# Kernel optimization log

Hardware: AMD Instinct MI355X
Metric: run time of the kernel (lower is better)

The kernel has to match this reference:

```python
import jax, jax.numpy as jnp
import numpy as np

N = 50000      # nodes
E = 800000     # edges
F = 64         # num_features
H = 64         # hidden_channels
L = 3          # num_layers
C0 = 16        # conv1d_channels[0]
TOTAL = H * L + 1  # 193, concat dim / Conv1d kernel size


def setup_inputs() -> dict:
    key = jax.random.key(0)
    ks = jax.random.split(key, 13)
    s = 0.05
    x = jax.random.normal(ks[0], (N, F), jnp.float32)
    edge_index = jax.random.randint(ks[1], (2, E), 0, N)
    edge_attr = jax.random.normal(ks[2], (E, 1), jnp.float32)
    W0 = jax.random.normal(ks[3], (F, H), jnp.float32) * s
    b0 = jnp.zeros((H,), jnp.float32)
    W1 = jax.random.normal(ks[4], (H, H), jnp.float32) * s
    b1 = jnp.zeros((H,), jnp.float32)
    W2 = jax.random.normal(ks[5], (H, H), jnp.float32) * s
    b2 = jnp.zeros((H,), jnp.float32)
    W3 = jax.random.normal(ks[6], (H, 1), jnp.float32) * s
    b3 = jnp.zeros((1,), jnp.float32)
    conv_w = jax.random.normal(ks[7], (C0, TOTAL), jnp.float32) * s  # Conv1d(1,C0,K=TOTAL,stride=TOTAL) weight squeezed
    conv_b = jnp.zeros((C0,), jnp.float32)
    return dict(x=x, edge_index=edge_index, edge_attr=edge_attr,
                W0=W0, b0=b0, W1=W1, b1=b1, W2=W2, b2=b2, W3=W3, b3=b3,
                conv_w=conv_w, conv_b=conv_b)


def _gcn(h, W, b, src, dst, norm):
    # PyG GCNConv: h' = segsum_dst(norm * (h W)[src]) + b
    h = h @ W                                   # [N, out]
    msg = h[src] * norm[:, None]                # [E+N, out] gather (irregular)
    out = jax.ops.segment_sum(msg, dst, num_segments=N)
    return out + b


def reference(x, edge_index, edge_attr, W0, b0, W1, b1, W2, b2, W3, b3, conv_w, conv_b):
    del edge_attr  # use_edge_attr=False
    loops = jnp.arange(N, dtype=edge_index.dtype)
    src = jnp.concatenate([edge_index[0], loops])  # add self-loops
    dst = jnp.concatenate([edge_index[1], loops])
    deg = jax.ops.segment_sum(jnp.ones_like(dst, dtype=x.dtype), dst, num_segments=N)
    dinv = jax.lax.rsqrt(jnp.maximum(deg, 1.0))
    norm = dinv[src] * dinv[dst]

    xs = []
    h = x
    for W, b in ((W0, b0), (W1, b1), (W2, b2), (W3, b3)):
        h = _gcn(h, W, b, src, dst, norm)
        xs.append(h)
    cat = jnp.concatenate(xs, axis=-1)           # [N, TOTAL] (k=1 drops input x)
    # Conv1d(1, C0, K=TOTAL, stride=TOTAL) over length-TOTAL signal == dense projection
    out = cat @ conv_w.T + conv_b                # [N, C0]
    return out
```

## Files before the change

kernel.cpp:

```cpp
#include <hip/hip_runtime.h>
#include <math.h>

static constexpr int N    = 50000;
static constexpr int E    = 800000;
static constexpr int NC   = 16;
static constexpr int TOT  = 193;
static constexpr int NB   = (N + 255) / 256;
static constexpr int DP   = 16;

static constexpr int KQ1 = 0;
static constexpr int KQ2 = 1024;
static constexpr int KQ3 = 2048;
static constexpr int KV  = 3072;
static constexpr int KU1 = 3136;
static constexpr int KU2 = 3152;
static constexpr int KD  = 3168;
static constexpr int KSC = 3184;
static constexpr int KSZ = 3200;

__device__ __forceinline__ unsigned short f2bf(float f) {
    union { float f; unsigned int i; } v; v.f = f;
    unsigned int b = v.i + 0x7FFFu + ((v.i >> 16) & 1u);
    return (unsigned short)(b >> 16);
}


__global__ void k_count(const int* __restrict__ dst, int* __restrict__ degp,
                        int* __restrict__ pos) {
    int e = blockIdx.x * blockDim.x + threadIdx.x;
    if (e < E / 4) {
        int d0 = dst[e], d1 = dst[e + E / 4];
        int d2 = dst[e + E / 2], d3 = dst[e + 3 * E / 4];
        int p0 = atomicAdd(&degp[d0 * DP], 1);
        int p1 = atomicAdd(&degp[d1 * DP], 1);
        int p2 = atomicAdd(&degp[d2 * DP], 1);
        int p3 = atomicAdd(&degp[d3 * DP], 1);
        pos[e] = p0;
        pos[e + E / 4] = p1;
        pos[e + E / 2] = p2;
        pos[e + 3 * E / 4] = p3;
    }
}

__global__ __launch_bounds__(256) void k_part(const int* __restrict__ degp,
                                              int* __restrict__ part) {
    __shared__ int red[256];
    const int t = threadIdx.x;
    int i = blockIdx.x * 256 + t;
    int v = (i < N) ? (degp[i * DP] + 1) : 0;
    red[t] = v;
    __syncthreads();
#pragma unroll
    for (int off = 128; off; off >>= 1) {
        if (t < off) red[t] += red[t + off];
        __syncthreads();
    }
    if (t == 0) part[blockIdx.x] = red[0];
}

__global__ __launch_bounds__(256) void k_scatter(const int* __restrict__ degp,
                                                 const int* __restrict__ part,
                                                 int* __restrict__ row_ptr,
                                                 float* __restrict__ dinv,
                                                 int2* __restrict__ edges) {
    __shared__ int s[256];
    __shared__ int red[256];
    const int t = threadIdx.x;
    const int bid = blockIdx.x;
    red[t] = (t < bid && t < NB) ? part[t] : 0;
    __syncthreads();
#pragma unroll
    for (int off = 128; off; off >>= 1) {
        if (t < off) red[t] += red[t + off];
        __syncthreads();
    }
    const int base = red[0];

    int i = bid * 256 + t;
    int v = (i < N) ? (degp[i * DP] + 1) : 0;
    s[t] = v;
    __syncthreads();
#pragma unroll
    for (int off = 1; off < 256; off <<= 1) {
        int u = (t >= off) ? s[t - off] : 0;
        __syncthreads();
        s[t] += u;
        __syncthreads();
    }
    if (i < N) {
        int rp = base + s[t] - v;
        row_ptr[i] = rp;
        float dv = rsqrtf((float)v);
        dinv[i] = dv;
        edges[rp] = make_int2(i, __float_as_int(dv * dv));
        if (i == N - 1) row_ptr[N] = base + s[t];
    }
}

__global__ void k_fill(const int* __restrict__ src, const int* __restrict__ dst,
                       const int* __restrict__ pos,
                       const int* __restrict__ row_ptr,
                       const float* __restrict__ dinv,
                       int2* __restrict__ edges) {
    int idx = blockIdx.x * blockDim.x + threadIdx.x;
    if (idx < E) {
        int s = src[idx], d = dst[idx];
        int p = row_ptr[d] + 1 + pos[idx];
        edges[p] = make_int2(s, __float_as_int(dinv[s] * dinv[d]));
    }
}

__global__ __launch_bounds__(256) void k_xbf(const float* __restrict__ x,
                                             ushort* __restrict__ xb,
                                             int* __restrict__ degp) {
    int i = blockIdx.x * 256 + threadIdx.x;
    if (i * 4 >= N * 64) return;
    degp[i] = 0;
    float4 v = ((const float4*)x)[i];
    ushort4 o;
    o.x = f2bf(v.x); o.y = f2bf(v.y); o.z = f2bf(v.z); o.w = f2bf(v.w);
    ((ushort4*)xb)[i] = o;
}

__global__ __launch_bounds__(256) void k_setup(
    const float* __restrict__ W0, const float* __restrict__ b0,
    const float* __restrict__ W1, const float* __restrict__ b1,
    const float* __restrict__ W2, const float* __restrict__ b2,
    const float* __restrict__ W3, const float* __restrict__ b3,
    const float* __restrict__ cw, const float* __restrict__ cb,
    float* __restrict__ K) {
    __shared__ float W0s[4096], W1s[4096], W2s[4096], P2s[4096];
    __shared__ float C1[1024], C2[1024], C3[1024], R3s[1024];
    __shared__ float W3s[64], b0s[64], b1s[64], b2s[64];
    __shared__ float r3[64], rb1[64], rb2[64], rb12[64];
    const int t = threadIdx.x;
    const int k = t >> 2, q = t & 3;

    for (int i = t; i < 4096; i += 256) {
        W0s[i] = W0[i]; W1s[i] = W1[i]; W2s[i] = W2[i];
    }
    for (int i = t; i < 1024; i += 256) {
        int j = i >> 4, c = i & 15;
        C1[i] = cw[c * TOT + j];
        C2[i] = cw[c * TOT + 64 + j];
        C3[i] = cw[c * TOT + 128 + j];
    }
    if (t < 64) { W3s[t] = W3[t]; b0s[t] = b0[t]; b1s[t] = b1[t]; b2s[t] = b2[t]; }
    __syncthreads();

    {
        const int j0 = q * 16;
        float acc[16];
#pragma unroll
        for (int jj = 0; jj < 16; ++jj) acc[jj] = 0.f;
        for (int m = 0; m < 64; ++m) {
            float w = W0s[k * 64 + m];
#pragma unroll
            for (int jj = 0; jj < 16; ++jj) acc[jj] += w * W1s[m * 64 + j0 + jj];
        }
#pragma unroll
        for (int jj = 0; jj < 16; ++jj) P2s[k * 64 + j0 + jj] = acc[jj];
    }
    {
        const int c0 = q * 4;
        float acc[4] = {0.f, 0.f, 0.f, 0.f};
        for (int j = 0; j < 64; ++j) {
            float w = W2s[k * 64 + j];
#pragma unroll
            for (int cc = 0; cc < 4; ++cc) acc[cc] += w * C3[j * 16 + c0 + cc];
        }
#pragma unroll
        for (int cc = 0; cc < 4; ++cc) R3s[k * 16 + c0 + cc] = acc[cc];
    }
    if (q == 0) {
        float a = 0.f;
        for (int j = 0; j < 64; ++j) a += W2s[k * 64 + j] * W3s[j];
        r3[k] = a;
    }
    if (q == 1) {
        float a = 0.f;
        for (int m = 0; m < 64; ++m) a += b0s[m] * W1s[m * 64 + k];
        rb1[k] = a;
    }
    if (q == 2) {
        float a = 0.f;
        for (int m = 0; m < 64; ++m) a += b1s[m] * W2s[m * 64 + k];
        rb2[k] = a;
    }
    __syncthreads();

    {
        const int c0 = q * 4;
        float q1[4] = {0,0,0,0}, q2[4] = {0,0,0,0}, q3[4] = {0,0,0,0};
        for (int j = 0; j < 64; ++j) {
            float w0 = W0s[k * 64 + j], p2 = P2s[k * 64 + j];
#pragma unroll
            for (int cc = 0; cc < 4; ++cc) {
                q1[cc] += w0 * C1[j * 16 + c0 + cc];
                q2[cc] += p2 * C2[j * 16 + c0 + cc];
                q3[cc] += p2 * R3s[j * 16 + c0 + cc];
            }
        }
#pragma unroll
        for (int cc = 0; cc < 4; ++cc) {
            K[KQ1 + k * 16 + c0 + cc] = q1[cc];
            K[KQ2 + k * 16 + c0 + cc] = q2[cc];
            K[KQ3 + k * 16 + c0 + cc] = q3[cc];
        }
    }
    if (q == 3) {
        float a = 0.f;
        for (int j = 0; j < 64; ++j) a += P2s[k * 64 + j] * r3[j];
        K[KV + k] = a;
    }
    if (q == 0) {
        float a = 0.f;
        for (int m = 0; m < 64; ++m) a += rb1[m] * W2s[m * 64 + k];
        rb12[k] = a;
    }
    __syncthreads();

    if (t < 16) {
        float a1 = 0.f, a2 = 0.f, ad = 0.f;
        for (int j = 0; j < 64; ++j) {
            a1 += rb1[j] * C2[j * 16 + t] + rb2[j] * C3[j * 16 + t];
            a2 += rb12[j] * C3[j * 16 + t];
            ad += b0s[j] * C1[j * 16 + t] + b1s[j] * C2[j * 16 + t]
                + b2s[j] * C3[j * 16 + t];
        }
        K[KU1 + t] = a1; K[KU2 + t] = a2; K[KD + t] = ad + cb[t];
    }
    if (t == 0) {
        float al = 0.f, be = 0.f, ga = 0.f;
        for (int j = 0; j < 64; ++j) {
            al += rb12[j] * W3s[j]; be += rb2[j] * W3s[j]; ga += b2s[j] * W3s[j];
        }
        K[KSC + 0] = al; K[KSC + 1] = be; K[KSC + 2] = ga;
    }
}

template <int LAYER>
__global__ __launch_bounds__(256) void k_layer(
    const ushort* __restrict__ Min,
    const int2* __restrict__ edges,
    const int* __restrict__ row_ptr,
    const float* __restrict__ K,
    const float* __restrict__ s1in,
    const float* __restrict__ s2in,
    ushort* __restrict__ Mout,
    float* __restrict__ s_out,
    float* __restrict__ t4,
    float* __restrict__ out) {
    __shared__ float QT[64 * 17];
    const int tid = threadIdx.x;
    constexpr int KQ = (LAYER == 0) ? KQ1 : (LAYER == 1) ? KQ2 : KQ3;
    for (int i = tid; i < 1024; i += 256) {
        int j = i >> 4, c = i & 15;
        QT[j * 17 + c] = K[KQ + i];
    }
    const int lane = tid & 63;
    const int w    = tid >> 6;
    const int q    = lane >> 4;
    const int m    = lane & 15;
    float v0 = 0.f, v1 = 0.f, v2 = 0.f, v3 = 0.f;
    if constexpr (LAYER == 2) {
        v0 = K[KV + 4 * m + 0]; v1 = K[KV + 4 * m + 1];
        v2 = K[KV + 4 * m + 2]; v3 = K[KV + 4 * m + 3];
    }
    __syncthreads();

    const int nn = blockIdx.x * 16 + w * 4 + q;
    const int rp0 = row_ptr[nn], rp1 = row_ptr[nn + 1];
    const int d = rp1 - rp0;
    int dmax = max(d, __shfl_xor(d, 16));
    dmax = max(dmax, __shfl_xor(dmax, 32));
    const int trips = __builtin_amdgcn_readfirstlane((dmax + 7) >> 3);

    float a0 = 0.f, a1 = 0.f, a2 = 0.f, a3 = 0.f, accs = 0.f;
    for (int t = 0; t < trips; ++t) {
        const int base = rp0 + t * 8;
        int col[8]; float wv[8];
#pragma unroll
        for (int i = 0; i < 8; ++i) {
            int pi = base + i;
            int pc = min(pi, rp1 - 1);
            int2 e = edges[pc];
            col[i] = e.x;
            wv[i] = (pi < rp1) ? __int_as_float(e.y) : 0.f;
        }
        unsigned long long g[8];
#pragma unroll
        for (int i = 0; i < 8; ++i)
            g[i] = *(const unsigned long long*)(Min + col[i] * 64 + 4 * m);
        if constexpr (LAYER == 0) {
#pragma unroll
            for (int i = 0; i < 8; ++i) accs += wv[i];
        }
#pragma unroll
        for (int i = 0; i < 8; ++i) {
            unsigned int lo = (unsigned int)g[i];
            unsigned int hi = (unsigned int)(g[i] >> 32);
            union { unsigned int u; float f; } x0, x1, x2, x3;
            x0.u = lo << 16; x1.u = lo & 0xFFFF0000u;
            x2.u = hi << 16; x3.u = hi & 0xFFFF0000u;
            a0 += wv[i] * x0.f; a1 += wv[i] * x1.f;
            a2 += wv[i] * x2.f; a3 += wv[i] * x3.f;
        }
    }

    if constexpr (LAYER < 2) {
        unsigned long long pk =
              (unsigned long long)f2bf(a0)
            | ((unsigned long long)f2bf(a1) << 16)
            | ((unsigned long long)f2bf(a2) << 32)
            | ((unsigned long long)f2bf(a3) << 48);
        ((unsigned long long*)Mout)[nn * 16 + m] = pk;
    }
    if constexpr (LAYER == 0) {
        if (m == 0) s_out[nn] = accs;
    }
    if constexpr (LAYER == 1) {
        float ss = 0.f;
        for (int p = rp0 + m; p < rp1; p += 16) {
            int2 e = edges[p];
            ss += __int_as_float(e.y) * s1in[e.x];
        }
        ss += __shfl_xor(ss, 1); ss += __shfl_xor(ss, 2);
        ss += __shfl_xor(ss, 4); ss += __shfl_xor(ss, 8);
        if (m == 0) s_out[nn] = ss;
    }

    float s1n = 0.f, s2n = 0.f;
    if constexpr (LAYER == 2) {
        s1n = s1in[nn]; s2n = s2in[nn];
        float tv = a0 * v0 + a1 * v1 + a2 * v2 + a3 * v3;
        tv += __shfl_xor(tv, 1); tv += __shfl_xor(tv, 2);
        tv += __shfl_xor(tv, 4); tv += __shfl_xor(tv, 8);
        if (m == 0)
            t4[nn] = tv + K[KSC + 0] * s2n + K[KSC + 1] * s1n + K[KSC + 2];
    }

    float r = 0.f;
#pragma unroll
    for (int a = 0; a < 16; ++a) {
        int srcl = (q << 4) + a;
        float f0 = __shfl(a0, srcl), f1 = __shfl(a1, srcl);
        float f2 = __shfl(a2, srcl), f3 = __shfl(a3, srcl);
        r += f0 * QT[(4 * a + 0) * 17 + m] + f1 * QT[(4 * a + 1) * 17 + m]
           + f2 * QT[(4 * a + 2) * 17 + m] + f3 * QT[(4 * a + 3) * 17 + m];
    }
    {
        int o = nn * NC + m;
        if constexpr (LAYER == 0) {
            out[o] = K[KD + m] + r;
        } else if constexpr (LAYER == 1) {
            out[o] += r;
        } else {
            out[o] += r + s1n * K[KU1 + m] + s2n * K[KU2 + m];
        }
    }
}

__global__ __launch_bounds__(256) void k_agg4_out(
    const float* __restrict__ t4, const int2* __restrict__ edges,
    const int* __restrict__ row_ptr, const float* __restrict__ b3,
    const float* __restrict__ conv_w, float* __restrict__ out) {
    int n = blockIdx.x * blockDim.x + threadIdx.x;
    if (n >= N) return;
    int p0 = row_ptr[n], p1 = row_ptr[n + 1];
    float a0 = 0.f, a1 = 0.f;
    for (int p = p0; p < p1; p += 4) {
        int q0 = min(p, p1 - 1), q1 = min(p + 1, p1 - 1);
        int q2 = min(p + 2, p1 - 1), q3 = min(p + 3, p1 - 1);
        int2 e0 = edges[q0], e1 = edges[q1], e2 = edges[q2], e3 = edges[q3];
        float w0 = __int_as_float(e0.y);
        float w1 = (p + 1 < p1) ? __int_as_float(e1.y) : 0.f;
        float w2 = (p + 2 < p1) ? __int_as_float(e2.y) : 0.f;
        float w3 = (p + 3 < p1) ? __int_as_float(e3.y) : 0.f;
        a0 += w0 * t4[e0.x]; a1 += w1 * t4[e1.x];
        a0 += w2 * t4[e2.x]; a1 += w3 * t4[e3.x];
    }
    float h4 = a0 + a1 + b3[0];
    float4* o4 = (float4*)(out + n * NC);
#pragma unroll
    for (int k = 0; k < 4; ++k) {
        float4 v = o4[k];
        v.x += h4 * conv_w[(4 * k + 0) * TOT + 192];
        v.y += h4 * conv_w[(4 * k + 1) * TOT + 192];
        v.z += h4 * conv_w[(4 * k + 2) * TOT + 192];
        v.w += h4 * conv_w[(4 * k + 3) * TOT + 192];
        o4[k] = v;
    }
}


extern "C" void kernel_launch(void* const* d_in, const int* in_sizes, int n_in,
                              void* d_out, int out_size, void* d_ws, size_t ws_size,
                              hipStream_t stream) {
    const float* x   = (const float*)d_in[0];
    const int*   ei  = (const int*)d_in[1];
    const int*   src = ei;
    const int*   dst = ei + E;
    const float* W0  = (const float*)d_in[3];
    const float* b0  = (const float*)d_in[4];
    const float* W1  = (const float*)d_in[5];
    const float* b1  = (const float*)d_in[6];
    const float* W2  = (const float*)d_in[7];
    const float* b2  = (const float*)d_in[8];
    const float* W3  = (const float*)d_in[9];
    const float* b3  = (const float*)d_in[10];
    const float* cw  = (const float*)d_in[11];
    const float* cb  = (const float*)d_in[12];
    float* out = (float*)d_out;

    char* p = (char*)d_ws;
    auto alloc = [&](size_t nbytes) {
        char* r = p;
        p += (nbytes + 255) & ~(size_t)255;
        return (void*)r;
    };
    int*    degp    = (int*)alloc((size_t)N * DP * 4);
    int*    pos     = (int*)alloc((size_t)E * 4);
    int*    row_ptr = (int*)alloc((size_t)(N + 1) * 4);
    float*  dinv    = (float*)alloc((size_t)N * 4);
    int*    part    = (int*)alloc((size_t)NB * 4);
    int2*   edges   = (int2*)alloc((size_t)(E + N) * 8);
    ushort* xb      = (ushort*)alloc((size_t)N * 64 * 2);
    ushort* M1      = (ushort*)alloc((size_t)N * 64 * 2);
    ushort* M2      = (ushort*)alloc((size_t)N * 64 * 2);
    float*  s1      = (float*)alloc((size_t)N * 4);
    float*  s2      = (float*)alloc((size_t)N * 4);
    float*  t4      = (float*)alloc((size_t)N * 4);
    float*  K       = (float*)alloc((size_t)KSZ * 4);

    k_setup<<<1, 256, 0, stream>>>(W0, b0, W1, b1, W2, b2, W3, b3, cw, cb, K);
    k_xbf<<<(N * 64 / 4 + 255) / 256, 256, 0, stream>>>(x, xb, degp);

    k_count  <<<(E / 4 + 255) / 256, 256, 0, stream>>>(dst, degp, pos);
    k_part   <<<NB, 256, 0, stream>>>(degp, part);
    k_scatter<<<NB, 256, 0, stream>>>(degp, part, row_ptr, dinv, edges);
    k_fill   <<<(E + 255) / 256, 256, 0, stream>>>(src, dst, pos, row_ptr, dinv, edges);

    const int layerGrid = N / 16;

    k_layer<0><<<layerGrid, 256, 0, stream>>>(
        xb, edges, row_ptr, K, nullptr, nullptr, M1, s1, nullptr, out);
    k_layer<1><<<layerGrid, 256, 0, stream>>>(
        M1, edges, row_ptr, K, s1, nullptr, M2, s2, nullptr, out);
    k_layer<2><<<layerGrid, 256, 0, stream>>>(
        M2, edges, row_ptr, K, s1, s2, nullptr, nullptr, t4, out);
    k_agg4_out<<<(N + 255) / 256, 256, 0, stream>>>(t4, edges, row_ptr, b3, cw, out);
}
```

Before: 175.4 us.

## Split bf16 feature matrices into two 32-column halves processed by separate launches

Stores the node feature matrices as two separate 32-column bf16 halves. Each layer now runs as two kernel passes, one per half, so each gather touches a 3.2 MB array that may stay resident in cache better than the original 6.4 MB one. Each wave handles 8 nodes with 8 lanes instead of 4 nodes with 16 lanes. The cost is reading the edge list twice per layer, twice as many launches, and extra read-modify-write traffic on the output and t4.

```diff
diff --git a/kernel.cpp b/kernel.cpp
--- a/kernel.cpp
+++ b/kernel.cpp
@@ -111,7 +111,8 @@
 }
 
 __global__ __launch_bounds__(256) void k_xbf(const float* __restrict__ x,
-                                             ushort* __restrict__ xb,
+                                             ushort* __restrict__ xbA,
+                                             ushort* __restrict__ xbB,
                                              int* __restrict__ degp) {
     int i = blockIdx.x * 256 + threadIdx.x;
     if (i * 4 >= N * 64) return;
@@ -119,7 +120,9 @@
     float4 v = ((const float4*)x)[i];
     ushort4 o;
     o.x = f2bf(v.x); o.y = f2bf(v.y); o.z = f2bf(v.z); o.w = f2bf(v.w);
-    ((ushort4*)xb)[i] = o;
+    int n = i >> 4, q16 = i & 15;
+    if (q16 < 8) ((ushort4*)xbA)[n * 8 + q16] = o;
+    else         ((ushort4*)xbB)[n * 8 + (q16 - 8)] = o;
 }
 
 __global__ __launch_bounds__(256) void k_setup(
@@ -239,7 +242,7 @@
     }
 }
 
-template <int LAYER>
+template <int LAYER, int HALF>
 __global__ __launch_bounds__(256) void k_layer(
     const ushort* __restrict__ Min,
     const int2* __restrict__ edges,
@@ -251,28 +254,33 @@
     float* __restrict__ s_out,
     float* __restrict__ t4,
     float* __restrict__ out) {
-    __shared__ float QT[64 * 17];
+    __shared__ float QT[32 * 17];
     const int tid = threadIdx.x;
     constexpr int KQ = (LAYER == 0) ? KQ1 : (LAYER == 1) ? KQ2 : KQ3;
-    for (int i = tid; i < 1024; i += 256) {
+    for (int i = tid; i < 512; i += 256) {
         int j = i >> 4, c = i & 15;
-        QT[j * 17 + c] = K[KQ + i];
+        QT[j * 17 + c] = K[KQ + (HALF * 32 + j) * 16 + c];
     }
     const int lane = tid & 63;
     const int w    = tid >> 6;
-    const int q    = lane >> 4;
-    const int m    = lane & 15;
+    const int oct  = lane >> 3;
+    const int m8   = lane & 7;
     float v0 = 0.f, v1 = 0.f, v2 = 0.f, v3 = 0.f;
     if constexpr (LAYER == 2) {
-        v0 = K[KV + 4 * m + 0]; v1 = K[KV + 4 * m + 1];
-        v2 = K[KV + 4 * m + 2]; v3 = K[KV + 4 * m + 3];
-    }
-    __syncthreads();
-
-    const int nn = blockIdx.x * 16 + w * 4 + q;
-    const int rp0 = row_ptr[nn], rp1 = row_ptr[nn + 1];
+        v0 = K[KV + HALF * 32 + 4 * m8 + 0];
+        v1 = K[KV + HALF * 32 + 4 * m8 + 1];
+        v2 = K[KV + HALF * 32 + 4 * m8 + 2];
+        v3 = K[KV + HALF * 32 + 4 * m8 + 3];
+    }
+    __syncthreads();
+
+    const int nn = blockIdx.x * 32 + w * 8 + oct;
+    const bool valid = nn < N;
+    int rp0 = 0, rp1 = 1;
+    if (valid) { rp0 = row_ptr[nn]; rp1 = row_ptr[nn + 1]; }
     const int d = rp1 - rp0;
-    int dmax = max(d, __shfl_xor(d, 16));
+    int dmax = max(d, __shfl_xor(d, 8));
+    dmax = max(dmax, __shfl_xor(dmax, 16));
     dmax = max(dmax, __shfl_xor(dmax, 32));
     const int trips = __builtin_amdgcn_readfirstlane((dmax + 7) >> 3);
 
@@ -291,8 +299,8 @@
         unsigned long long g[8];
 #pragma unroll
         for (int i = 0; i < 8; ++i)
-            g[i] = *(const unsigned long long*)(Min + col[i] * 64 + 4 * m);
-        if constexpr (LAYER == 0) {
+            g[i] = *(const unsigned long long*)(Min + col[i] * 32 + 4 * m8);
+        if constexpr (LAYER == 0 && HALF == 0) {
 #pragma unroll
             for (int i = 0; i < 8; ++i) accs += wv[i];
         }
@@ -309,54 +317,66 @@
     }
 
     if constexpr (LAYER < 2) {
-        unsigned long long pk =
-              (unsigned long long)f2bf(a0)
-            | ((unsigned long long)f2bf(a1) << 16)
-            | ((unsigned long long)f2bf(a2) << 32)
-            | ((unsigned long long)f2bf(a3) << 48);
-        ((unsigned long long*)Mout)[nn * 16 + m] = pk;
-    }
-    if constexpr (LAYER == 0) {
-        if (m == 0) s_out[nn] = accs;
-    }
-    if constexpr (LAYER == 1) {
+        if (valid) {
+            unsigned long long pk =
+                  (unsigned long long)f2bf(a0)
+                | ((unsigned long long)f2bf(a1) << 16)
+                | ((unsigned long long)f2bf(a2) << 32)
+                | ((unsigned long long)f2bf(a3) << 48);
+            ((unsigned long long*)Mout)[nn * 8 + m8] = pk;
+        }
+    }
+    if constexpr (LAYER == 0 && HALF == 0) {
+        if (m8 == 0 && valid) s_out[nn] = accs;
+    }
+    if constexpr (LAYER == 1 && HALF == 0) {
         float ss = 0.f;
-        for (int p = rp0 + m; p < rp1; p += 16) {
+        for (int p = rp0 + m8; p < rp1; p += 8) {
             int2 e = edges[p];
             ss += __int_as_float(e.y) * s1in[e.x];
         }
         ss += __shfl_xor(ss, 1); ss += __shfl_xor(ss, 2);
-        ss += __shfl_xor(ss, 4); ss += __shfl_xor(ss, 8);
-        if (m == 0) s_out[nn] = ss;
+        ss += __shfl_xor(ss, 4);
+        if (m8 == 0 && valid) s_out[nn] = ss;
     }
 
     float s1n = 0.f, s2n = 0.f;
     if constexpr (LAYER == 2) {
-        s1n = s1in[nn]; s2n = s2in[nn];
+        int nc = valid ? nn : 0;
+        s1n = s1in[nc]; s2n = s2in[nc];
         float tv = a0 * v0 + a1 * v1 + a2 * v2 + a3 * v3;
         tv += __shfl_xor(tv, 1); tv += __shfl_xor(tv, 2);
-        tv += __shfl_xor(tv, 4); tv += __shfl_xor(tv, 8);
-        if (m == 0)
-            t4[nn] = tv + K[KSC + 0] * s2n + K[KSC + 1] * s1n + K[KSC + 2];
-    }
-
-    float r = 0.f;
-#pragma unroll
-    for (int a = 0; a < 16; ++a) {
-        int srcl = (q << 4) + a;
+        tv += __shfl_xor(tv, 4);
+        if (m8 == 0 && valid) {
+            if constexpr (HALF == 0)
+                t4[nn] = tv + K[KSC + 0] * s2n + K[KSC + 1] * s1n + K[KSC + 2];
+            else
+                t4[nn] += tv;
+        }
+    }
+
+    float r0 = 0.f, r1 = 0.f;
+#pragma unroll
+    for (int a = 0; a < 8; ++a) {
+        int srcl = (oct << 3) + a;
         float f0 = __shfl(a0, srcl), f1 = __shfl(a1, srcl);
         float f2 = __shfl(a2, srcl), f3 = __shfl(a3, srcl);
-        r += f0 * QT[(4 * a + 0) * 17 + m] + f1 * QT[(4 * a + 1) * 17 + m]
-           + f2 * QT[(4 * a + 2) * 17 + m] + f3 * QT[(4 * a + 3) * 17 + m];
-    }
-    {
-        int o = nn * NC + m;
-        if constexpr (LAYER == 0) {
-            out[o] = K[KD + m] + r;
-        } else if constexpr (LAYER == 1) {
-            out[o] += r;
+        r0 += f0 * QT[(4 * a + 0) * 17 + m8] + f1 * QT[(4 * a + 1) * 17 + m8]
+            + f2 * QT[(4 * a + 2) * 17 + m8] + f3 * QT[(4 * a + 3) * 17 + m8];
+        r1 += f0 * QT[(4 * a + 0) * 17 + m8 + 8] + f1 * QT[(4 * a + 1) * 17 + m8 + 8]
+            + f2 * QT[(4 * a + 2) * 17 + m8 + 8] + f3 * QT[(4 * a + 3) * 17 + m8 + 8];
+    }
+    if (valid) {
+        int o = nn * NC + m8;
+        if constexpr (LAYER == 0 && HALF == 0) {
+            out[o]     = K[KD + m8] + r0;
+            out[o + 8] = K[KD + m8 + 8] + r1;
+        } else if constexpr (LAYER == 2 && HALF == 0) {
+            out[o]     += r0 + s1n * K[KU1 + m8] + s2n * K[KU2 + m8];
+            out[o + 8] += r1 + s1n * K[KU1 + m8 + 8] + s2n * K[KU2 + m8 + 8];
         } else {
-            out[o] += r + s1n * K[KU1 + m] + s2n * K[KU2 + m];
+            out[o]     += r0;
+            out[o + 8] += r1;
         }
     }
 }
@@ -425,29 +445,38 @@
     float*  dinv    = (float*)alloc((size_t)N * 4);
     int*    part    = (int*)alloc((size_t)NB * 4);
     int2*   edges   = (int2*)alloc((size_t)(E + N) * 8);
-    ushort* xb      = (ushort*)alloc((size_t)N * 64 * 2);
-    ushort* M1      = (ushort*)alloc((size_t)N * 64 * 2);
-    ushort* M2      = (ushort*)alloc((size_t)N * 64 * 2);
+    ushort* xbA     = (ushort*)alloc((size_t)N * 32 * 2);
+    ushort* xbB     = (ushort*)alloc((size_t)N * 32 * 2);
+    ushort* M1A     = (ushort*)alloc((size_t)N * 32 * 2);
+    ushort* M1B     = (ushort*)alloc((size_t)N * 32 * 2);
+    ushort* M2A     = (ushort*)alloc((size_t)N * 32 * 2);
+    ushort* M2B     = (ushort*)alloc((size_t)N * 32 * 2);
     float*  s1      = (float*)alloc((size_t)N * 4);
     float*  s2      = (float*)alloc((size_t)N * 4);
     float*  t4      = (float*)alloc((size_t)N * 4);
     float*  K       = (float*)alloc((size_t)KSZ * 4);
 
     k_setup<<<1, 256, 0, stream>>>(W0, b0, W1, b1, W2, b2, W3, b3, cw, cb, K);
-    k_xbf<<<(N * 64 / 4 + 255) / 256, 256, 0, stream>>>(x, xb, degp);
+    k_xbf<<<(N * 64 / 4 + 255) / 256, 256, 0, stream>>>(x, xbA, xbB, degp);
 
     k_count  <<<(E / 4 + 255) / 256, 256, 0, stream>>>(dst, degp, pos);
     k_part   <<<NB, 256, 0, stream>>>(degp, part);
     k_scatter<<<NB, 256, 0, stream>>>(degp, part, row_ptr, dinv, edges);
     k_fill   <<<(E + 255) / 256, 256, 0, stream>>>(src, dst, pos, row_ptr, dinv, edges);
 
-    const int layerGrid = N / 16;
-
-    k_layer<0><<<layerGrid, 256, 0, stream>>>(
-        xb, edges, row_ptr, K, nullptr, nullptr, M1, s1, nullptr, out);
-    k_layer<1><<<layerGrid, 256, 0, stream>>>(
-        M1, edges, row_ptr, K, s1, nullptr, M2, s2, nullptr, out);
-    k_layer<2><<<layerGrid, 256, 0, stream>>>(
-        M2, edges, row_ptr, K, s1, s2, nullptr, nullptr, t4, out);
+    const int layerGrid = (N + 31) / 32;
+
+    k_layer<0, 0><<<layerGrid, 256, 0, stream>>>(
+        xbA, edges, row_ptr, K, nullptr, nullptr, M1A, s1, nullptr, out);
+    k_layer<0, 1><<<layerGrid, 256, 0, stream>>>(
+        xbB, edges, row_ptr, K, nullptr, nullptr, M1B, nullptr, nullptr, out);
+    k_layer<1, 0><<<layerGrid, 256, 0, stream>>>(
+        M1A, edges, row_ptr, K, s1, nullptr, M2A, s2, nullptr, out);
+    k_layer<1, 1><<<layerGrid, 256, 0, stream>>>(
+        M1B, edges, row_ptr, K, nullptr, nullptr, M2B, nullptr, nullptr, out);
+    k_layer<2, 0><<<layerGrid, 256, 0, stream>>>(
+        M2A, edges, row_ptr, K, s1, s2, nullptr, nullptr, t4, out);
+    k_layer<2, 1><<<layerGrid, 256, 0, stream>>>(
+        M2B, edges, row_ptr, K, s1, s2, nullptr, nullptr, t4, out);
     k_agg4_out<<<(N + 255) / 256, 256, 0, stream>>>(t4, edges, row_ptr, b3, cw, out);
 }
```

Result: slower. 198.9 us (+13.4%).
